# Performance work log

Hardware: AMD Instinct MI355X
Metric: run time of the kernel (lower is better)

## Reference

```python
import jax, jax.numpy as jnp
import numpy as np
import math

BS, S, D_IN, D_OUT, RANK = 4, 2048, 4096, 4096, 128
BASE_LR = 0.01
EPS = 1e-6
SQRT_IN = math.sqrt(D_IN)  # scalar_scaler


def setup_inputs() -> dict:
    key = jax.random.key(0)
    ks = jax.random.split(key, 8)
    return {
        "x": jax.random.normal(ks[0], (BS, S, D_IN), dtype=jnp.float32),
        "log_lr": jax.random.normal(ks[1], (RANK, D_IN), dtype=jnp.float32) * 0.01,
        "state": jax.random.normal(ks[2], (BS, RANK, D_IN), dtype=jnp.float32) * 0.02,
        "grad_buffer": jax.random.normal(ks[3], (BS, RANK, D_IN), dtype=jnp.float32) * 0.01,
        "w_bsp": jax.random.normal(ks[4], (RANK, D_IN), dtype=jnp.float32) * 0.02,
        "w_out": jax.random.normal(ks[5], (D_OUT, RANK), dtype=jnp.float32) * 0.02,
        "w_lin": jax.random.normal(ks[6], (D_OUT, D_IN), dtype=jnp.float32) * 0.02,
        "b_lin": jnp.zeros((D_OUT,), dtype=jnp.float32),
    }


def reference(x, log_lr, state, grad_buffer, w_bsp, w_out, w_lin, b_lin):
    # lr = base_lr * exp(log_lr * sqrt(in_features))  -> [rank, in]
    lr = BASE_LR * jnp.exp(log_lr * SQRT_IN)
    # s = lr[None] * state  -> [bs, rank, in]; state is detached in the original
    s = lr[None] * state
    # z = einsum('boi,bsi->bso', s, x)  -> [bs, seq, rank]
    z = jnp.einsum("bri,bsi->bsr", s, x)
    # FoItttFunction.apply is identity on z in the forward
    # z + base_state_proj(x)
    z = z + jnp.einsum("bsi,ri->bsr", x, w_bsp)
    # out_proj(z) + linear(x)
    y = jnp.einsum("bsr,or->bso", z, w_out) + jnp.einsum("bsi,oi->bso", x, w_lin) + b_lin
    return y
```

## Files before the change

kernel.cpp:

```cpp
#include <hip/hip_runtime.h>
#include <hip/hip_bf16.h>

typedef __attribute__((ext_vector_type(8))) short bf16x8;
typedef __attribute__((ext_vector_type(4))) float f32x4;

#define DEVI static __device__ __forceinline__

constexpr int BS = 4, SEQ = 2048, DIN = 4096, DOUT = 4096, RANK = 128;
constexpr int MTOT = BS * SEQ;

DEVI unsigned short f2bf(float f) {
  __hip_bfloat16 h = __float2bfloat16(f);
  return __builtin_bit_cast(unsigned short, h);
}


__global__ void cast_bf16_kernel(const float* __restrict__ src,
                                 unsigned short* __restrict__ dst, int n4) {
  int i = blockIdx.x * blockDim.x + threadIdx.x;
  int stride = gridDim.x * blockDim.x;
  for (; i < n4; i += stride) {
    float4 v = reinterpret_cast<const float4*>(src)[i];
    ushort4 o;
    o.x = f2bf(v.x); o.y = f2bf(v.y); o.z = f2bf(v.z); o.w = f2bf(v.w);
    reinterpret_cast<ushort4*>(dst)[i] = o;
  }
}

__global__ void prep_m_kernel(const float* __restrict__ log_lr,
                              const float* __restrict__ state,
                              const float* __restrict__ w_bsp,
                              unsigned short* __restrict__ m_bf) {
  const int n4 = BS * RANK * DIN / 4;
  int i = blockIdx.x * blockDim.x + threadIdx.x;
  int stride = gridDim.x * blockDim.x;
  for (; i < n4; i += stride) {
    int ri4 = (i * 4) % (RANK * DIN) / 4;
    float4 ll = reinterpret_cast<const float4*>(log_lr)[ri4];
    float4 wb = reinterpret_cast<const float4*>(w_bsp)[ri4];
    float4 st = reinterpret_cast<const float4*>(state)[i];
    ushort4 o;
    o.x = f2bf(0.01f * __expf(ll.x * 64.0f) * st.x + wb.x);
    o.y = f2bf(0.01f * __expf(ll.y * 64.0f) * st.y + wb.y);
    o.z = f2bf(0.01f * __expf(ll.z * 64.0f) * st.z + wb.z);
    o.w = f2bf(0.01f * __expf(ll.w * 64.0f) * st.w + wb.w);
    reinterpret_cast<ushort4*>(m_bf)[i] = o;
  }
}


DEVI void gload16(const void* g, void* l) {
  __builtin_amdgcn_global_load_lds(
      (const __attribute__((address_space(1))) void*)g,
      (__attribute__((address_space(3))) void*)l, 16, 0, 0);
}

template <int ROWS>
DEVI void stage_tile(const char* gbase, int ldBytes, char* lds) {
  const int lane = threadIdx.x & 63;
  const int wave = threadIdx.x >> 6;
  constexpr int CHUNKS = ROWS / 16;
  constexpr int CPW = CHUNKS / 4;
  const int colByte = (lane & 3) << 4;
  const int rowInChunk = lane >> 2;
#pragma unroll
  for (int c = 0; c < CPW; ++c) {
    int chunk = wave * CPW + c;
    int row = chunk * 16 + rowInChunk;
    gload16(gbase + (size_t)row * ldBytes + colByte, lds + chunk * 1024);
  }
}

template <int F>
DEVI void compute_tile(const char* lA, const char* lB, f32x4 (&acc)[F][F]) {
  const int lane = threadIdx.x & 63;
  const int wave = threadIdx.x >> 6;
  const int wr = wave >> 1, wc = wave & 1;
  const int kByte = (lane >> 4) * 16;
  const int rsel = lane & 15;
  bf16x8 a[F], b[F];
#pragma unroll
  for (int mi = 0; mi < F; ++mi) {
    int row = wr * (F * 16) + mi * 16 + rsel;
    a[mi] = *reinterpret_cast<const bf16x8*>(lA + row * 64 + kByte);
  }
#pragma unroll
  for (int ni = 0; ni < F; ++ni) {
    int row = wc * (F * 16) + ni * 16 + rsel;
    b[ni] = *reinterpret_cast<const bf16x8*>(lB + row * 64 + kByte);
  }
#pragma unroll
  for (int mi = 0; mi < F; ++mi)
#pragma unroll
    for (int ni = 0; ni < F; ++ni)
      acc[mi][ni] =
          __builtin_amdgcn_mfma_f32_16x16x32_bf16(a[mi], b[ni], acc[mi][ni], 0, 0, 0);
}

__global__ __launch_bounds__(256) void z_gemm_kernel(
    const unsigned short* __restrict__ xbf, const unsigned short* __restrict__ mbf,
    unsigned short* __restrict__ zbf) {
  int mt = blockIdx.x >> 1, nt = blockIdx.x & 1;
  int row0 = mt * 64;
  int batch = row0 >> 11;
  const char* xb = (const char*)(xbf + (size_t)row0 * DIN);
  const char* mb = (const char*)(mbf + ((size_t)batch * RANK + nt * 64) * DIN);
  __shared__ __align__(16) char lA[2][64 * 64];
  __shared__ __align__(16) char lB[2][64 * 64];
  f32x4 acc[2][2] = {};
  constexpr int NT = DIN / 32;
  stage_tile<64>(xb, DIN * 2, lA[0]);
  stage_tile<64>(mb, DIN * 2, lB[0]);
  for (int t = 0; t < NT; ++t) {
    __syncthreads();
    if (t + 1 < NT) {
      stage_tile<64>(xb + (t + 1) * 64, DIN * 2, lA[(t + 1) & 1]);
      stage_tile<64>(mb + (t + 1) * 64, DIN * 2, lB[(t + 1) & 1]);
    }
    compute_tile<2>(lA[t & 1], lB[t & 1], acc);
  }
  const int lane = threadIdx.x & 63;
  const int wave = threadIdx.x >> 6;
  const int wr = wave >> 1, wc = wave & 1;
#pragma unroll
  for (int mi = 0; mi < 2; ++mi)
#pragma unroll
    for (int ni = 0; ni < 2; ++ni) {
      int c = nt * 64 + wc * 32 + ni * 16 + (lane & 15);
      int r0 = row0 + wr * 32 + mi * 16 + (lane >> 4) * 4;
#pragma unroll
      for (int j = 0; j < 4; ++j)
        zbf[(size_t)(r0 + j) * RANK + c] = f2bf(acc[mi][ni][j]);
    }
}

__global__ __launch_bounds__(256) void main_gemm_kernel(
    const unsigned short* __restrict__ xbf, const unsigned short* __restrict__ wlbf,
    const unsigned short* __restrict__ zbf, const unsigned short* __restrict__ wobf,
    const float* __restrict__ b_lin, float* __restrict__ out) {
  int bid = blockIdx.x;
  int swz = (bid & 7) * 256 + (bid >> 3);
  int mt = swz >> 5, nt = swz & 31;
  int row0 = mt * 128, col0 = nt * 128;

  const char* xb = (const char*)(xbf + (size_t)row0 * DIN);
  const char* wb = (const char*)(wlbf + (size_t)col0 * DIN);
  const char* zb = (const char*)(zbf + (size_t)row0 * RANK);
  const char* ob = (const char*)(wobf + (size_t)col0 * RANK);

  __shared__ __align__(16) char lA[2][128 * 64];
  __shared__ __align__(16) char lB[2][128 * 64];
  f32x4 acc[4][4] = {};

  constexpr int NK1 = DIN / 32;
  constexpr int NK2 = RANK / 32;
  constexpr int NT = NK1 + NK2;

  stage_tile<128>(xb, DIN * 2, lA[0]);
  stage_tile<128>(wb, DIN * 2, lB[0]);

  for (int t = 0; t < NT; ++t) {
    __syncthreads();
    int nx = t + 1;
    if (nx < NT) {
      char* dA = lA[nx & 1];
      char* dB = lB[nx & 1];
      if (nx < NK1) {
        stage_tile<128>(xb + nx * 64, DIN * 2, dA);
        stage_tile<128>(wb + nx * 64, DIN * 2, dB);
      } else {
        int kb = (nx - NK1) * 64;
        stage_tile<128>(zb + kb, RANK * 2, dA);
        stage_tile<128>(ob + kb, RANK * 2, dB);
      }
    }
    compute_tile<4>(lA[t & 1], lB[t & 1], acc);
  }

  const int lane = threadIdx.x & 63;
  const int wave = threadIdx.x >> 6;
  const int wr = wave >> 1, wc = wave & 1;
  const int rbase = row0 + wr * 64 + (lane >> 4) * 4;
  const int cbase = col0 + wc * 64 + (lane & 15);
#pragma unroll
  for (int mi = 0; mi < 4; ++mi)
#pragma unroll
    for (int ni = 0; ni < 4; ++ni) {
      int c = cbase + ni * 16;
      float bv = b_lin[c];
      int r = rbase + mi * 16;
#pragma unroll
      for (int j = 0; j < 4; ++j)
        out[(size_t)(r + j) * DOUT + c] = acc[mi][ni][j] + bv;
    }
}


extern "C" void kernel_launch(void* const* d_in, const int* in_sizes, int n_in,
                              void* d_out, int out_size, void* d_ws, size_t ws_size,
                              hipStream_t stream) {
  const float* x = (const float*)d_in[0];
  const float* log_lr = (const float*)d_in[1];
  const float* state = (const float*)d_in[2];
  const float* w_bsp = (const float*)d_in[4];
  const float* w_out = (const float*)d_in[5];
  const float* w_lin = (const float*)d_in[6];
  const float* b_lin = (const float*)d_in[7];
  float* out = (float*)d_out;

  unsigned short* xbf = (unsigned short*)d_ws;
  unsigned short* wlbf = xbf + (size_t)MTOT * DIN;
  unsigned short* wobf = wlbf + (size_t)DOUT * DIN;
  unsigned short* mbf = wobf + (size_t)DOUT * RANK;
  unsigned short* zbf = mbf + (size_t)BS * RANK * DIN;

  cast_bf16_kernel<<<2048, 256, 0, stream>>>(x, xbf, MTOT * DIN / 4);
  cast_bf16_kernel<<<2048, 256, 0, stream>>>(w_lin, wlbf, DOUT * DIN / 4);
  cast_bf16_kernel<<<512, 256, 0, stream>>>(w_out, wobf, DOUT * RANK / 4);
  prep_m_kernel<<<2048, 256, 0, stream>>>(log_lr, state, w_bsp, mbf);
  z_gemm_kernel<<<256, 256, 0, stream>>>(xbf, mbf, zbf);
  main_gemm_kernel<<<2048, 256, 0, stream>>>(xbf, wlbf, zbf, wobf, b_lin, out);
}
```

Measured before the change: 671.8 us.

## Use 256x256 eight-wave main GEMM with swizzled LDS and split-K z GEMM

Replaces the 128x128 main GEMM with a 256x256-tile, 512-thread kernel. It uses XOR-swizzled LDS staging, a finer-grained phase schedule that interleaves global-to-LDS loads with MFMA, and s_setprio to raise priority during the MFMA bursts. The z GEMM, which had only 256 blocks, gets a split-K variant over 4 K-slices plus a reduction kernel to fill more CUs, used when the workspace is large enough. The bigger tiles cut global re-reads of x and w_lin, at the cost of 128KB LDS per block and more register pressure.

```diff
diff --git a/kernel.cpp b/kernel.cpp
--- a/kernel.cpp
+++ b/kernel.cpp
@@ -95,6 +95,65 @@
     for (int ni = 0; ni < F; ++ni)
       acc[mi][ni] =
           __builtin_amdgcn_mfma_f32_16x16x32_bf16(a[mi], b[ni], acc[mi][ni], 0, 0, 0);
+}
+
+template <int KS>
+__global__ __launch_bounds__(256) void z_gemm_splitk(
+    const unsigned short* __restrict__ xbf, const unsigned short* __restrict__ mbf,
+    float* __restrict__ zpart) {
+  int bid = blockIdx.x;
+  int ksl = bid & (KS - 1);
+  int rest = bid / KS;
+  int nt = rest & 1, mt = rest >> 1;
+  int row0 = mt * 64;
+  int batch = row0 >> 11;
+  int kbase = ksl * (DIN / KS);
+  const char* xb = (const char*)(xbf + (size_t)row0 * DIN + kbase);
+  const char* mb = (const char*)(mbf + ((size_t)batch * RANK + nt * 64) * DIN + kbase);
+  __shared__ __align__(16) char lA[2][64 * 64];
+  __shared__ __align__(16) char lB[2][64 * 64];
+  f32x4 acc[2][2] = {};
+  constexpr int NT = DIN / KS / 32;
+  stage_tile<64>(xb, DIN * 2, lA[0]);
+  stage_tile<64>(mb, DIN * 2, lB[0]);
+  for (int t = 0; t < NT; ++t) {
+    __syncthreads();
+    if (t + 1 < NT) {
+      stage_tile<64>(xb + (t + 1) * 64, DIN * 2, lA[(t + 1) & 1]);
+      stage_tile<64>(mb + (t + 1) * 64, DIN * 2, lB[(t + 1) & 1]);
+    }
+    compute_tile<2>(lA[t & 1], lB[t & 1], acc);
+  }
+  const int lane = threadIdx.x & 63;
+  const int wave = threadIdx.x >> 6;
+  const int wr = wave >> 1, wc = wave & 1;
+#pragma unroll
+  for (int mi = 0; mi < 2; ++mi)
+#pragma unroll
+    for (int ni = 0; ni < 2; ++ni) {
+      int c = nt * 64 + wc * 32 + ni * 16 + (lane & 15);
+      int r0 = row0 + wr * 32 + mi * 16 + (lane >> 4) * 4;
+#pragma unroll
+      for (int j = 0; j < 4; ++j)
+        zpart[((size_t)ksl * MTOT + r0 + j) * RANK + c] = acc[mi][ni][j];
+    }
+}
+
+template <int KS>
+__global__ void z_reduce_kernel(const float* __restrict__ zpart,
+                                unsigned short* __restrict__ zbf) {
+  const int n4 = MTOT * RANK / 4;
+  int i = blockIdx.x * blockDim.x + threadIdx.x;
+  if (i >= n4) return;
+  float4 s = reinterpret_cast<const float4*>(zpart)[i];
+#pragma unroll
+  for (int k = 1; k < KS; ++k) {
+    float4 v = reinterpret_cast<const float4*>(zpart)[(size_t)k * n4 + i];
+    s.x += v.x; s.y += v.y; s.z += v.z; s.w += v.w;
+  }
+  ushort4 o;
+  o.x = f2bf(s.x); o.y = f2bf(s.y); o.z = f2bf(s.z); o.w = f2bf(s.w);
+  reinterpret_cast<ushort4*>(zbf)[i] = o;
 }
 
 __global__ __launch_bounds__(256) void z_gemm_kernel(
@@ -134,64 +193,140 @@
     }
 }
 
-__global__ __launch_bounds__(256) void main_gemm_kernel(
+
+struct MainCtx {
+  const char* lds;
+  int wr, wc, rsel, kgrp, xorv;
+};
+
+DEVI const bf16x8* lda_frag(const MainCtx& c, int d, int mi, int ks) {
+  int col = ((ks * 64) + c.kgrp * 16) ^ c.xorv;
+  return reinterpret_cast<const bf16x8*>(
+      c.lds + d * 32768 + c.wr * 16384 + mi * 2048 + c.rsel * 128 + col);
+}
+DEVI const bf16x8* ldb_frag(const MainCtx& c, int d, int ni, int ks) {
+  int col = ((ks * 64) + c.kgrp * 16) ^ c.xorv;
+  return reinterpret_cast<const bf16x8*>(
+      c.lds + 65536 + d * 32768 + (c.wc >> 1) * 16384 + (c.wc & 1) * 8192 +
+      ni * 2048 + c.rsel * 128 + col);
+}
+
+template <int D, int Q, class STG>
+DEVI void phase_body(const MainCtx& c, f32x4 (&acc)[8][4], bf16x8 (&bfr)[4][2],
+                     STG&& stg) {
+  bf16x8 a00 = *lda_frag(c, D, 2 * Q, 0);
+  bf16x8 a01 = *lda_frag(c, D, 2 * Q, 1);
+  bf16x8 a10 = *lda_frag(c, D, 2 * Q + 1, 0);
+  bf16x8 a11 = *lda_frag(c, D, 2 * Q + 1, 1);
+  if (Q == 0) {
+#pragma unroll
+    for (int ni = 0; ni < 4; ++ni) {
+      bfr[ni][0] = *ldb_frag(c, D, ni, 0);
+      bfr[ni][1] = *ldb_frag(c, D, ni, 1);
+    }
+  }
+  stg();
+  __builtin_amdgcn_s_barrier();
+  asm volatile("s_waitcnt lgkmcnt(0)" ::: "memory");
+  __builtin_amdgcn_s_setprio(1);
+#pragma unroll
+  for (int ni = 0; ni < 4; ++ni) {
+    acc[2 * Q][ni] = __builtin_amdgcn_mfma_f32_16x16x32_bf16(a00, bfr[ni][0], acc[2 * Q][ni], 0, 0, 0);
+    acc[2 * Q + 1][ni] = __builtin_amdgcn_mfma_f32_16x16x32_bf16(a10, bfr[ni][0], acc[2 * Q + 1][ni], 0, 0, 0);
+  }
+#pragma unroll
+  for (int ni = 0; ni < 4; ++ni) {
+    acc[2 * Q][ni] = __builtin_amdgcn_mfma_f32_16x16x32_bf16(a01, bfr[ni][1], acc[2 * Q][ni], 0, 0, 0);
+    acc[2 * Q + 1][ni] = __builtin_amdgcn_mfma_f32_16x16x32_bf16(a11, bfr[ni][1], acc[2 * Q + 1][ni], 0, 0, 0);
+  }
+  __builtin_amdgcn_s_setprio(0);
+  asm volatile("s_waitcnt vmcnt(4)" ::: "memory");
+  __builtin_amdgcn_s_barrier();
+}
+
+__global__ __launch_bounds__(512, 2) void main_gemm_8p(
     const unsigned short* __restrict__ xbf, const unsigned short* __restrict__ wlbf,
     const unsigned short* __restrict__ zbf, const unsigned short* __restrict__ wobf,
     const float* __restrict__ b_lin, float* __restrict__ out) {
+  __shared__ __align__(16) char lds[131072];
+
+  const int tid = threadIdx.x;
+  const int lane = tid & 63, wave = tid >> 6;
+
   int bid = blockIdx.x;
-  int swz = (bid & 7) * 256 + (bid >> 3);
-  int mt = swz >> 5, nt = swz & 31;
-  int row0 = mt * 128, col0 = nt * 128;
+  int swz = (bid & 7) * 64 + (bid >> 3);
+  int mt = swz >> 4, nt = swz & 15;
+  const int row0 = mt * 256, col0 = nt * 256;
 
   const char* xb = (const char*)(xbf + (size_t)row0 * DIN);
   const char* wb = (const char*)(wlbf + (size_t)col0 * DIN);
   const char* zb = (const char*)(zbf + (size_t)row0 * RANK);
   const char* ob = (const char*)(wobf + (size_t)col0 * RANK);
 
-  __shared__ __align__(16) char lA[2][128 * 64];
-  __shared__ __align__(16) char lB[2][128 * 64];
-  f32x4 acc[4][4] = {};
-
-  constexpr int NK1 = DIN / 32;
-  constexpr int NK2 = RANK / 32;
-  constexpr int NT = NK1 + NK2;
-
-  stage_tile<128>(xb, DIN * 2, lA[0]);
-  stage_tile<128>(wb, DIN * 2, lB[0]);
-
-  for (int t = 0; t < NT; ++t) {
-    __syncthreads();
-    int nx = t + 1;
-    if (nx < NT) {
-      char* dA = lA[nx & 1];
-      char* dB = lB[nx & 1];
-      if (nx < NK1) {
-        stage_tile<128>(xb + nx * 64, DIN * 2, dA);
-        stage_tile<128>(wb + nx * 64, DIN * 2, dB);
-      } else {
-        int kb = (nx - NK1) * 64;
-        stage_tile<128>(zb + kb, RANK * 2, dA);
-        stage_tile<128>(ob + kb, RANK * 2, dB);
-      }
-    }
-    compute_tile<4>(lA[t & 1], lB[t & 1], acc);
-  }
-
-  const int lane = threadIdx.x & 63;
-  const int wave = threadIdx.x >> 6;
-  const int wr = wave >> 1, wc = wave & 1;
-  const int rbase = row0 + wr * 64 + (lane >> 4) * 4;
+  const int srow8 = lane >> 3;
+  const int scolS = ((lane & 7) ^ srow8) << 4;
+  const int chunk0 = wave * 2;
+
+  auto stage = [&](const char* gbase, int ld, int ldsOff) {
+    gload16(gbase + (size_t)(chunk0 * 8 + srow8) * ld + scolS,
+            (void*)&lds[ldsOff + chunk0 * 1024]);
+    gload16(gbase + (size_t)(chunk0 * 8 + 8 + srow8) * ld + scolS,
+            (void*)&lds[ldsOff + chunk0 * 1024 + 1024]);
+  };
+  auto stageA = [&](int k, int h, int d) {
+    const char* g; int ld;
+    if (k < 64) { g = xb + (size_t)h * 128 * (DIN * 2) + (size_t)k * 128; ld = DIN * 2; }
+    else        { g = zb + (size_t)h * 128 * (RANK * 2) + (size_t)(k - 64) * 128; ld = RANK * 2; }
+    stage(g, ld, d * 32768 + h * 16384);
+  };
+  auto stageB = [&](int k, int h, int d) {
+    const char* g; int ld;
+    if (k < 64) { g = wb + (size_t)h * 128 * (DIN * 2) + (size_t)k * 128; ld = DIN * 2; }
+    else        { g = ob + (size_t)h * 128 * (RANK * 2) + (size_t)(k - 64) * 128; ld = RANK * 2; }
+    stage(g, ld, 65536 + d * 32768 + h * 16384);
+  };
+
+  MainCtx c{lds, wave >> 2, wave & 3, lane & 15, lane >> 4, (lane & 7) << 4};
+
+  f32x4 acc[8][4] = {};
+  bf16x8 bfr[4][2];
+
+  stageB(0, 0, 0); stageB(0, 1, 0);
+  stageA(0, 0, 0); stageA(0, 1, 0);
+  stageB(1, 0, 1); stageB(1, 1, 1);
+  asm volatile("s_waitcnt vmcnt(4)" ::: "memory");
+  __builtin_amdgcn_s_barrier();
+
+  constexpr int NKT = 66;
+  for (int j = 0; j < NKT / 2; ++j) {
+    int t = 2 * j;
+    int kA1 = (t + 1 < NKT - 1) ? t + 1 : NKT - 1;
+    int kN2 = (t + 2 < NKT - 1) ? t + 2 : NKT - 1;
+    int kB3 = (t + 3 < NKT - 1) ? t + 3 : NKT - 1;
+    phase_body<0, 0>(c, acc, bfr, [&] { stageA(kA1, 0, 1); });
+    phase_body<0, 1>(c, acc, bfr, [&] { stageA(kA1, 1, 1); });
+    phase_body<0, 2>(c, acc, bfr, [&] { stageB(kN2, 0, 0); });
+    phase_body<0, 3>(c, acc, bfr, [&] { stageB(kN2, 1, 0); });
+    phase_body<1, 0>(c, acc, bfr, [&] { stageA(kN2, 0, 0); });
+    phase_body<1, 1>(c, acc, bfr, [&] { stageA(kN2, 1, 0); });
+    phase_body<1, 2>(c, acc, bfr, [&] { stageB(kB3, 0, 1); });
+    phase_body<1, 3>(c, acc, bfr, [&] { stageB(kB3, 1, 1); });
+  }
+  asm volatile("s_waitcnt vmcnt(0)" ::: "memory");
+
+  const int wr = wave >> 2, wc = wave & 3;
+  const int rbase = row0 + wr * 128 + (lane >> 4) * 4;
   const int cbase = col0 + wc * 64 + (lane & 15);
 #pragma unroll
-  for (int mi = 0; mi < 4; ++mi)
+  for (int mi = 0; mi < 8; ++mi)
 #pragma unroll
     for (int ni = 0; ni < 4; ++ni) {
-      int c = cbase + ni * 16;
-      float bv = b_lin[c];
+      int cc = cbase + ni * 16;
+      float bv = b_lin[cc];
       int r = rbase + mi * 16;
 #pragma unroll
-      for (int j = 0; j < 4; ++j)
-        out[(size_t)(r + j) * DOUT + c] = acc[mi][ni][j] + bv;
+      for (int j2 = 0; j2 < 4; ++j2)
+        out[(size_t)(r + j2) * DOUT + cc] = acc[mi][ni][j2] + bv;
     }
 }
 
@@ -213,11 +348,20 @@
   unsigned short* wobf = wlbf + (size_t)DOUT * DIN;
   unsigned short* mbf = wobf + (size_t)DOUT * RANK;
   unsigned short* zbf = mbf + (size_t)BS * RANK * DIN;
+  float* zpart = (float*)(zbf + (size_t)MTOT * RANK);
+  const size_t need_split = 108003328 + 16777216;
 
   cast_bf16_kernel<<<2048, 256, 0, stream>>>(x, xbf, MTOT * DIN / 4);
   cast_bf16_kernel<<<2048, 256, 0, stream>>>(w_lin, wlbf, DOUT * DIN / 4);
   cast_bf16_kernel<<<512, 256, 0, stream>>>(w_out, wobf, DOUT * RANK / 4);
   prep_m_kernel<<<2048, 256, 0, stream>>>(log_lr, state, w_bsp, mbf);
-  z_gemm_kernel<<<256, 256, 0, stream>>>(xbf, mbf, zbf);
-  main_gemm_kernel<<<2048, 256, 0, stream>>>(xbf, wlbf, zbf, wobf, b_lin, out);
-}
+
+  if (ws_size >= need_split) {
+    z_gemm_splitk<4><<<1024, 256, 0, stream>>>(xbf, mbf, zpart);
+    z_reduce_kernel<4><<<1024, 256, 0, stream>>>(zpart, zbf);
+  } else {
+    z_gemm_kernel<<<256, 256, 0, stream>>>(xbf, mbf, zbf);
+  }
+
+  main_gemm_8p<<<512, 512, 0, stream>>>(xbf, wlbf, zbf, wobf, b_lin, out);
+}
```

Measured after the change: 563.2 us. -16.2%, faster.
